# Optimization experiments

Hardware: AMD Instinct MI355X
Metric: run time of the kernel (lower is better)

## Reference

```python
import jax, jax.numpy as jnp
import numpy as np

D = 4096          # input_dims
P = 1             # p in Get_Atten_map_mc
NUM_IMG = 16
N_PER = 64        # objects per image
R_PER = 512       # relations per image
LN_EPS = 1e-5


def _linear_params(key, out_dim, in_dim):
    kw, kb = jax.random.split(key)
    w = jax.random.normal(kw, (out_dim, in_dim), jnp.float32) * 0.02
    b = jax.random.normal(kb, (out_dim,), jnp.float32) * 0.02
    return w, b


def setup_inputs() -> dict:
    key = jax.random.key(0)
    ks = jax.random.split(key, 12)
    N = NUM_IMG * N_PER
    R = NUM_IMG * R_PER

    obj_feats = jax.random.normal(ks[0], (N, D), jnp.float32)
    phr_feats = jax.random.normal(ks[1], (R, D), jnp.float32)

    # im_inds: uniform N_PER objects per image
    im_inds = jnp.repeat(jnp.arange(NUM_IMG, dtype=jnp.int64), N_PER)

    # rel_inds: [img_idx, subj_global, obj_global], R_PER rels per image,
    # subject/object indices local-to-image then offset to global ids.
    subj_loc = jax.random.randint(ks[2], (NUM_IMG, R_PER), 0, N_PER)
    obj_loc = jax.random.randint(ks[3], (NUM_IMG, R_PER), 0, N_PER)
    offs = (jnp.arange(NUM_IMG) * N_PER)[:, None]
    img_col = jnp.repeat(jnp.arange(NUM_IMG), R_PER)
    rel_inds = jnp.stack(
        [img_col, (subj_loc + offs).reshape(-1), (obj_loc + offs).reshape(-1)], axis=1
    ).astype(jnp.int64)

    Ws_w, Ws_b = _linear_params(ks[4], D, D)       # ws
    Wo_w, Wo_b = _linear_params(ks[5], D, D)       # wo
    Ww_w, Ww_b = _linear_params(ks[6], P, D)       # w (attention logits)
    Wc_w, Wc_b = _linear_params(ks[7], D // 2, D)  # conv Linear
    Wt1_w, Wt1_b = _linear_params(ks[8], D // 4, D)
    Wt2_w, Wt2_b = _linear_params(ks[9], D, D // 4)
    ln_g = jnp.ones((D // 4,), jnp.float32)
    ln_b = jnp.zeros((D // 4,), jnp.float32)

    return {
        "obj_feats": obj_feats, "phr_feats": phr_feats,
        "im_inds": im_inds, "rel_inds": rel_inds, "num_img": NUM_IMG,
        "Ws_w": Ws_w, "Ws_b": Ws_b, "Wo_w": Wo_w, "Wo_b": Wo_b,
        "Ww_w": Ww_w, "Ww_b": Ww_b, "Wc_w": Wc_w, "Wc_b": Wc_b,
        "Wt1_w": Wt1_w, "Wt1_b": Wt1_b, "ln_g": ln_g, "ln_b": ln_b,
        "Wt2_w": Wt2_w, "Wt2_b": Wt2_b,
    }


def reference(obj_feats, phr_feats, im_inds, rel_inds, num_img,
              Ws_w, Ws_b, Wo_w, Wo_b, Ww_w, Ww_b, Wc_w, Wc_b,
              Wt1_w, Wt1_b, ln_g, ln_b, Wt2_w, Wt2_b):
    N, d = obj_feats.shape
    n_per = N // num_img
    R = rel_inds.shape[0]
    r_per = R // num_img
    p = Ww_w.shape[0]

    # ws/wo projections over all objects (original recomputes them per image
    # on the full obj_feats -- identical math, computed once here).
    ws_all = obj_feats @ Ws_w.T + Ws_b
    wo_all = obj_feats @ Wo_w.T + Wo_b

    subj = rel_inds[:, 1]
    objc = rel_inds[:, 2]
    prod = ws_all[subj] * wo_all[objc]               # [R, D]
    atten_f = (prod * phr_feats) @ Ww_w.T + Ww_b     # [R, p]

    # conv on object features
    conv_all = jax.nn.relu(obj_feats @ Wc_w.T + Wc_b)  # [N, D/2]

    subj_i = subj.reshape(num_img, r_per)
    objc_i = objc.reshape(num_img, r_per)
    af_i = atten_f.reshape(num_img, r_per, p)
    conv_i = conv_all.reshape(num_img, n_per, -1)

    self_mask = 1.0 - jnp.eye(n_per, dtype=jnp.float32)[:, :, None]  # [n,n,1]

    def per_image(s, o, af, conv_feats):
        head = jnp.minimum(s.min(), o.min())
        A = jnp.zeros((n_per, n_per, p), jnp.float32).at[s - head, o - head].add(af)
        A = jax.nn.sigmoid(A) * self_mask
        A = A / A.sum(1)                               # [n,n,p] / [n,p] (col-normalize)
        A2 = jnp.concatenate([A, A.transpose(1, 0, 2)], axis=-1)  # [n,n,2p]
        # mc_matmul: concat of per-channel mm -> channel-major reshape
        return jnp.einsum('ijc,jd->icd', A2, conv_feats).reshape(n_per, -1)

    ctx = jax.vmap(per_image)(subj_i, objc_i, af_i, conv_i)  # [num_img, n, 2p*D/2]
    ctx = ctx.reshape(N, -1)                                  # [N, D]

    # trans: Linear -> LayerNorm -> ReLU -> Linear
    h = ctx @ Wt1_w.T + Wt1_b
    mu = h.mean(-1, keepdims=True)
    var = ((h - mu) ** 2).mean(-1, keepdims=True)
    h = (h - mu) * jax.lax.rsqrt(var + LN_EPS) * ln_g + ln_b
    h = jax.nn.relu(h)
    out = h @ Wt2_w.T + Wt2_b

    return jax.nn.relu(obj_feats + out)
```

## Files before the change

### kernel.cpp

```cpp
#include <hip/hip_runtime.h>
#include <hip/hip_bf16.h>
#include <math.h>

#define D_   4096
#define NIMG 16
#define NPER 64
#define RPER 512
#define NTOT 1024
#define RTOT 8192
#define DC   2048
#define DT   1024
#define LDW  8192

typedef __attribute__((ext_vector_type(4))) float f32x4;
typedef __attribute__((ext_vector_type(8))) short bf16x8;

#define GLD16(gp, lp) __builtin_amdgcn_global_load_lds( \
    (const __attribute__((address_space(1))) unsigned int*)(gp), \
    (__attribute__((address_space(3))) unsigned int*)(lp), 16, 0, 0)

template<int N> __device__ __forceinline__ void waitvm() {
    asm volatile("s_waitcnt vmcnt(%0)" :: "n"(N) : "memory");
}

__device__ __forceinline__ void fma4(float4& d, float s, const float4 c) {
    d.x = fmaf(s, c.x, d.x); d.y = fmaf(s, c.y, d.y);
    d.z = fmaf(s, c.z, d.z); d.w = fmaf(s, c.w, d.w);
}
__device__ __forceinline__ void st4bf(__hip_bfloat16* p, float4 v) {
    union { __hip_bfloat16 h[4]; ushort4 u; } cv;
    cv.h[0] = __float2bfloat16(v.x); cv.h[1] = __float2bfloat16(v.y);
    cv.h[2] = __float2bfloat16(v.z); cv.h[3] = __float2bfloat16(v.w);
    *(ushort4*)p = cv.u;
}
__device__ __forceinline__ float bf2f(ushort u) {
    union { float f; unsigned int i; } c; c.i = (unsigned int)u << 16; return c.f;
}

__global__ __launch_bounds__(256) void cast_all(
    const float* __restrict__ obj, __hip_bfloat16* __restrict__ obj_bf,
    const float* __restrict__ Ws, const float* __restrict__ Wo,
    const float* __restrict__ Wc, __hip_bfloat16* __restrict__ wbuf,
    const float* __restrict__ Wt1, __hip_bfloat16* __restrict__ wt1r,
    const float* __restrict__ Wt2, __hip_bfloat16* __restrict__ wt2b,
    const float* __restrict__ b0, const float* __restrict__ b1,
    const float* __restrict__ b2, float* __restrict__ cb)
{
    const int b = blockIdx.x;
    const int t = threadIdx.x;
    if (b >= 26624) {
        const int i = (b - 26624) * 256 + t;
        float v;
        if (i < 4096) v = b0[i];
        else if (i < 8192) v = b1[i - 4096];
        else v = b2[i - 8192];
        cb[i] = v;
        return;
    }
    const float* s; __hip_bfloat16* d;
    if (b < 2048)       { s = obj + (size_t)b * 2048;            d = obj_bf + (size_t)b * 2048; }
    else if (b < 10240) { const int rb = b - 2048;  s = Ws + (size_t)rb * 2048; d = wbuf + (size_t)rb * 2048; }
    else if (b < 18432) { const int rb = b - 10240; s = Wo + (size_t)rb * 2048; d = wbuf + 16777216 + (size_t)rb * 2048; }
    else if (b < 22528) { const int rb = b - 18432; s = Wc + (size_t)rb * 2048; d = wbuf + 33554432 + (size_t)rb * 2048; }
    else if (b < 24576) { const int r = b - 22528;
                          s = Wt1 + (size_t)(r & 1023) * 4096 + (r >> 10) * 2048;
                          d = wt1r + (size_t)r * 2048; }
    else                { const int rb = b - 24576; s = Wt2 + (size_t)rb * 2048; d = wt2b + (size_t)rb * 2048; }
    const int i = t * 8;
    float4 v0 = *(const float4*)(s + i);
    float4 v1 = *(const float4*)(s + i + 4);
    union { __hip_bfloat16 h[8]; ushort4 u[2]; } cv;
    cv.h[0] = __float2bfloat16(v0.x); cv.h[1] = __float2bfloat16(v0.y);
    cv.h[2] = __float2bfloat16(v0.z); cv.h[3] = __float2bfloat16(v0.w);
    cv.h[4] = __float2bfloat16(v1.x); cv.h[5] = __float2bfloat16(v1.y);
    cv.h[6] = __float2bfloat16(v1.z); cv.h[7] = __float2bfloat16(v1.w);
    *(ushort4*)(d + i)     = cv.u[0];
    *(ushort4*)(d + i + 4) = cv.u[1];
}

template<int BM, int BN>
__global__ __launch_bounds__(256) void gemm_p2(
    const ushort* __restrict__ A, const ushort* __restrict__ B,
    const float* __restrict__ bias, const float* __restrict__ resid,
    float* __restrict__ C, __hip_bfloat16* __restrict__ C2,
    __hip_bfloat16* __restrict__ C3,
    int M, int K, int ldc, int mode)
{
    constexpr int MREP = BM / 32;
    constexpr int NREP = BN / 32;
    constexpr int SLOTS = (BM + BN) * 4;
    constexpr int NPW = SLOTS / 256;
    constexpr int BUFE = SLOTS * 8;

    __shared__ ushort lds[3][BUFE];

    const int t = threadIdx.x;
    const int lane = t & 63;
    const int wid = t >> 6;
    const int wr = wid >> 1, wc = wid & 1;

    const int MT = M / BM;
    const int G = gridDim.x;
    const int bid = blockIdx.x;
    const int wgid = (bid & 7) * (G >> 3) + (bid >> 3);
    const int nt = wgid / MT, mt = wgid % MT;
    const int bm = mt * BM, bn = nt * BN;

    const ushort* gp[NPW];
    int loff[NPW];
#pragma unroll
    for (int i = 0; i < NPW; ++i) {
        const int slot = i * 256 + t;
        const bool isA = slot < BM * 4;
        const int s2 = isA ? slot : slot - BM * 4;
        const int row = s2 >> 2;
        const int q = (s2 & 3) ^ ((row >> 1) & 3);
        gp[i] = (isA ? A + (size_t)(bm + row) * K : B + (size_t)(bn + row) * K) + q * 8;
        loff[i] = slot * 8;
    }

    auto stage = [&](int b, int kpos) {
#pragma unroll
        for (int i = 0; i < NPW; ++i) GLD16(gp[i] + kpos, &lds[b][loff[i]]);
    };

    int aoff[MREP], boff[NREP];
    const int sx = (((lane >> 4) ^ ((lane >> 1) & 3))) << 3;
#pragma unroll
    for (int m = 0; m < MREP; ++m)
        aoff[m] = (wr * (BM / 2) + (lane & 15) + m * 16) * 32 + sx;
#pragma unroll
    for (int n = 0; n < NREP; ++n)
        boff[n] = BM * 32 + (wc * (BN / 2) + (lane & 15) + n * 16) * 32 + sx;

    f32x4 acc[MREP][NREP] = {};

    const int NT = K >> 5;
    stage(0, 0);
    stage(1, 32);
    if constexpr (NPW == 2) waitvm<2>();
    else if constexpr (NPW == 3) waitvm<3>();
    else waitvm<4>();
    __builtin_amdgcn_sched_barrier(0);
    __builtin_amdgcn_s_barrier();
    __builtin_amdgcn_sched_barrier(0);

    for (int tt = 0; tt < NT; ++tt) {
        const bool pf = (tt + 2 < NT);
        if (pf) stage((tt + 2) % 3, (tt + 2) << 5);
        __builtin_amdgcn_sched_barrier(0);

        const ushort* lb = lds[tt % 3];
        bf16x8 af[MREP], bfv[NREP];
#pragma unroll
        for (int m = 0; m < MREP; ++m) af[m] = *(const bf16x8*)(lb + aoff[m]);
#pragma unroll
        for (int n = 0; n < NREP; ++n) bfv[n] = *(const bf16x8*)(lb + boff[n]);
#pragma unroll
        for (int m = 0; m < MREP; ++m)
#pragma unroll
            for (int n = 0; n < NREP; ++n)
                acc[m][n] = __builtin_amdgcn_mfma_f32_16x16x32_bf16(
                    af[m], bfv[n], acc[m][n], 0, 0, 0);

        __builtin_amdgcn_sched_barrier(0);
        if (pf) {
            if constexpr (NPW == 2) waitvm<2>();
            else if constexpr (NPW == 3) waitvm<3>();
            else waitvm<4>();
        } else {
            waitvm<0>();
        }
        __builtin_amdgcn_sched_barrier(0);
        __builtin_amdgcn_s_barrier();
        __builtin_amdgcn_sched_barrier(0);
    }

    const int col0 = bn + wc * (BN / 2) + (lane & 15);
    const int row0 = bm + wr * (BM / 2) + ((lane >> 4) << 2);
#pragma unroll
    for (int m = 0; m < MREP; ++m) {
#pragma unroll
        for (int n = 0; n < NREP; ++n) {
            const int cn = col0 + n * 16;
            const float bz = bias ? bias[cn] : 0.f;
#pragma unroll
            for (int rg = 0; rg < 4; ++rg) {
                const int gm = row0 + m * 16 + rg;
                float v = acc[m][n][rg] + bz;
                if (mode == 2) {
                    C[(size_t)gm * ldc + cn] = fmaxf(v + resid[(size_t)gm * ldc + cn], 0.f);
                } else if (mode == 4) {
                    if (cn < 8192)
                        C2[(size_t)gm * LDW + cn] = __float2bfloat16(v);
                    else
                        C3[(size_t)gm * 2048 + (cn - 8192)] =
                            __float2bfloat16(fmaxf(v, 0.f));
                } else {
                    C[(size_t)gm * ldc + cn] = v;
                }
            }
        }
    }
}

__global__ __launch_bounds__(256) void atten_kernel(
    const ushort* __restrict__ wswo, const float* __restrict__ phr,
    const int* __restrict__ rel, const float* __restrict__ Www,
    const float* __restrict__ Wwb, float* __restrict__ atten)
{
    const int r = blockIdx.x;
    const int s = rel[r * 3 + 1], o = rel[r * 3 + 2];
    const int t = threadIdx.x;
    const ushort* pws = wswo + (size_t)s * LDW;
    const ushort* pwo = wswo + (size_t)o * LDW + 4096;
    const float*  pph = phr + (size_t)r * D_;
    float sum = 0.f;
#pragma unroll
    for (int half = 0; half < 2; ++half) {
        const int q = t * 8 + half * 2048;
        ushort4 w0 = *(const ushort4*)(pws + q);
        ushort4 w1 = *(const ushort4*)(pws + q + 4);
        ushort4 u0 = *(const ushort4*)(pwo + q);
        ushort4 u1 = *(const ushort4*)(pwo + q + 4);
        float4 p0 = *(const float4*)(pph + q);
        float4 p1 = *(const float4*)(pph + q + 4);
        float4 g0 = *(const float4*)(Www + q);
        float4 g1 = *(const float4*)(Www + q + 4);
        sum += bf2f(w0.x) * bf2f(u0.x) * p0.x * g0.x
             + bf2f(w0.y) * bf2f(u0.y) * p0.y * g0.y
             + bf2f(w0.z) * bf2f(u0.z) * p0.z * g0.z
             + bf2f(w0.w) * bf2f(u0.w) * p0.w * g0.w
             + bf2f(w1.x) * bf2f(u1.x) * p1.x * g1.x
             + bf2f(w1.y) * bf2f(u1.y) * p1.y * g1.y
             + bf2f(w1.z) * bf2f(u1.z) * p1.z * g1.z
             + bf2f(w1.w) * bf2f(u1.w) * p1.w * g1.w;
    }
    for (int off = 32; off > 0; off >>= 1) sum += __shfl_down(sum, off);
    __shared__ float red[4];
    if ((t & 63) == 0) red[t >> 6] = sum;
    __syncthreads();
    if (t == 0) atten[r] = red[0] + red[1] + red[2] + red[3] + Wwb[0];
}

__global__ __launch_bounds__(256) void build_A(
    const int* __restrict__ rel, const float* __restrict__ atten,
    float* __restrict__ Anorm)
{
    const int g = blockIdx.x;
    const int t = threadIdx.x;
    __shared__ float Am[64][64];
    __shared__ float S[64];
    __shared__ int headSh;
    for (int i = t; i < 4096; i += 256) ((float*)Am)[i] = 0.f;
    if (t == 0) headSh = 0x7fffffff;

    int lmin = 0x7fffffff;
    for (int rr = t; rr < RPER; rr += 256) {
        const int base = (g * RPER + rr) * 3;
        lmin = min(lmin, min(rel[base + 1], rel[base + 2]));
    }
    for (int off = 32; off > 0; off >>= 1) lmin = min(lmin, __shfl_down(lmin, off));
    __syncthreads();
    if ((t & 63) == 0) atomicMin(&headSh, lmin);
    __syncthreads();
    const int head = headSh;

    for (int rr = t; rr < RPER; rr += 256) {
        const int base = (g * RPER + rr) * 3;
        atomicAdd(&Am[rel[base + 1] - head][rel[base + 2] - head],
                  atten[g * RPER + rr]);
    }
    __syncthreads();

    for (int idx = t; idx < 4096; idx += 256) {
        const int i = idx >> 6, j = idx & 63;
        float v = 1.f / (1.f + expf(-Am[i][j]));
        if (i == j) v = 0.f;
        Am[i][j] = v;
    }
    __syncthreads();

    if (t < 64) {
        float sum = 0.f;
        for (int k = 0; k < 64; ++k) sum += Am[t][k];
        S[t] = sum;
    }
    __syncthreads();

    float* outg = Anorm + (size_t)g * 4096;
    for (int idx = t; idx < 4096; idx += 256) {
        const int j = idx & 63;
        outg[idx] = ((const float*)Am)[idx] / S[j];
    }
}

__global__ __launch_bounds__(256) void amult_ln(
    const float* __restrict__ Anorm, const float* __restrict__ P,
    const float* __restrict__ w1b, const float* __restrict__ gamma,
    const float* __restrict__ beta, __hip_bfloat16* __restrict__ hb)
{
    const int g = blockIdx.x >> 6;
    const int i = blockIdx.x & 63;
    const int t = threadIdx.x;
    __shared__ float Ar[64], Ac[64];
    if (t < 64) Ar[t] = Anorm[(size_t)g * 4096 + i * 64 + t];
    else if (t < 128) { const int j = t - 64; Ac[j] = Anorm[(size_t)g * 4096 + j * 64 + i]; }
    __syncthreads();

    const float* pg = P + (size_t)g * 64 * 2048;
    float4 v = {0, 0, 0, 0};
    for (int j = 0; j < 64; ++j) {
        float4 p1 = *(const float4*)(pg + (size_t)j * 2048 + (t << 2));
        float4 p2 = *(const float4*)(pg + (size_t)j * 2048 + 1024 + (t << 2));
        fma4(v, Ar[j], p1);
        fma4(v, Ac[j], p2);
    }
    float4 b0 = *(const float4*)(w1b + (t << 2));
    v.x += b0.x; v.y += b0.y; v.z += b0.z; v.w += b0.w;

    float s  = v.x + v.y + v.z + v.w;
    float ss = v.x * v.x + v.y * v.y + v.z * v.z + v.w * v.w;
    for (int off = 32; off > 0; off >>= 1) {
        s  += __shfl_down(s, off);
        ss += __shfl_down(ss, off);
    }
    __shared__ float rs[4], rss[4];
    if ((t & 63) == 0) { rs[t >> 6] = s; rss[t >> 6] = ss; }
    __syncthreads();
    const float tot  = rs[0] + rs[1] + rs[2] + rs[3];
    const float tot2 = rss[0] + rss[1] + rss[2] + rss[3];
    const float mu   = tot * (1.f / DT);
    const float var  = tot2 * (1.f / DT) - mu * mu;
    const float rstd = rsqrtf(var + 1e-5f);
    float4 g4 = *(const float4*)(gamma + (t << 2));
    float4 b4 = *(const float4*)(beta + (t << 2));
    float4 o;
    o.x = fmaxf(fmaf((v.x - mu) * rstd, g4.x, b4.x), 0.f);
    o.y = fmaxf(fmaf((v.y - mu) * rstd, g4.y, b4.y), 0.f);
    o.z = fmaxf(fmaf((v.z - mu) * rstd, g4.z, b4.z), 0.f);
    o.w = fmaxf(fmaf((v.w - mu) * rstd, g4.w, b4.w), 0.f);
    st4bf(hb + (size_t)(g * 64 + i) * DT + (t << 2), o);
}

extern "C" void kernel_launch(void* const* d_in, const int* in_sizes, int n_in,
                              void* d_out, int out_size, void* d_ws, size_t ws_size,
                              hipStream_t stream)
{
    const float* obj   = (const float*)d_in[0];
    const float* phr   = (const float*)d_in[1];
    const int*   rel   = (const int*)d_in[3];
    const float* Ws_w  = (const float*)d_in[5];
    const float* Ws_b  = (const float*)d_in[6];
    const float* Wo_w  = (const float*)d_in[7];
    const float* Wo_b  = (const float*)d_in[8];
    const float* Ww_w  = (const float*)d_in[9];
    const float* Ww_b  = (const float*)d_in[10];
    const float* Wc_w  = (const float*)d_in[11];
    const float* Wc_b  = (const float*)d_in[12];
    const float* Wt1_w = (const float*)d_in[13];
    const float* Wt1_b = (const float*)d_in[14];
    const float* ln_g  = (const float*)d_in[15];
    const float* ln_b  = (const float*)d_in[16];
    const float* Wt2_w = (const float*)d_in[17];
    const float* Wt2_b = (const float*)d_in[18];
    float* out = (float*)d_out;

    float* ws = (float*)d_ws;
    __hip_bfloat16* wbuf    = (__hip_bfloat16*)ws;
    __hip_bfloat16* h_bf    = (__hip_bfloat16*)ws;
    __hip_bfloat16* obj_bf  = (__hip_bfloat16*)(ws + 20971520);
    float* Pbuf             = ws + 20971520;
    __hip_bfloat16* wswo_bf = (__hip_bfloat16*)(ws + 23068672);
    __hip_bfloat16* conv_bf = (__hip_bfloat16*)(ws + 27262976);
    __hip_bfloat16* wt1r    = (__hip_bfloat16*)(ws + 28311552);
    __hip_bfloat16* wt2b    = (__hip_bfloat16*)(ws + 30408704);
    float* atten  = ws + 32505856;
    float* Anorm  = ws + 32514048;
    float* cbias  = ws + 32579584;

    const dim3 blk(256);

    cast_all<<<dim3(26664), blk, 0, stream>>>(
        obj, obj_bf, Ws_w, Wo_w, Wc_w, wbuf, Wt1_w, wt1r, Wt2_w, wt2b,
        Ws_b, Wo_b, Wc_b, cbias);

    gemm_p2<128, 128><<<dim3(640), blk, 0, stream>>>(
        (const ushort*)obj_bf, (const ushort*)wbuf, cbias, nullptr,
        nullptr, wswo_bf, conv_bf, NTOT, D_, 0, 4);

    atten_kernel<<<dim3(RTOT), blk, 0, stream>>>(
        (const ushort*)wswo_bf, phr, rel, Ww_w, Ww_b, atten);
    build_A<<<dim3(NIMG), blk, 0, stream>>>(rel, atten, Anorm);

    gemm_p2<64, 64><<<dim3(512), blk, 0, stream>>>(
        (const ushort*)conv_bf, (const ushort*)wt1r, nullptr, nullptr,
        Pbuf, nullptr, nullptr, NTOT, DC, DC, 0);

    amult_ln<<<dim3(1024), blk, 0, stream>>>(Anorm, Pbuf, Wt1_b, ln_g, ln_b, h_bf);

    gemm_p2<64, 128><<<dim3(512), blk, 0, stream>>>(
        (const ushort*)h_bf, (const ushort*)wt2b, Wt2_b, obj,
        out, nullptr, nullptr, NTOT, DT, D_, 2);
}
```

Before: 299.1 us.

## Stage mode-4 GEMM epilogue through LDS for vectorized bf16 stores; remap blocks across XCDs

In the fused GEMM's mode-4 epilogue, each wave writes its bias-added (and ReLU'd) bf16 tile into a padded LDS patch, then reads it back row-wise and writes 16-byte vectors to global memory instead of scattered 2-byte stores. The atten and amult_ln kernels remap blockIdx so consecutive relation/image work lands on the same XCD (mod-8 interleave), aiming for better L2 locality on the gathered rows. The LDS staging reuses the GEMM's LDS buffer and assumes it is large enough and no longer needed. The XCD remap assumes round-robin dispatch across 8 XCDs.

```diff
diff --git a/kernel.cpp b/kernel.cpp
--- a/kernel.cpp
+++ b/kernel.cpp
@@ -35,6 +35,9 @@
 }
 __device__ __forceinline__ float bf2f(ushort u) {
     union { float f; unsigned int i; } c; c.i = (unsigned int)u << 16; return c.f;
+}
+__device__ __forceinline__ ushort f2bfu(float v) {
+    union { __hip_bfloat16 h; ushort u; } c; c.h = __float2bfloat16(v); return c.u;
 }
 
 __global__ __launch_bounds__(256) void cast_all(
@@ -178,6 +181,43 @@
 
     const int col0 = bn + wc * (BN / 2) + (lane & 15);
     const int row0 = bm + wr * (BM / 2) + ((lane >> 4) << 2);
+
+    if (mode == 4) {
+        ushort* patch = ((ushort*)lds) + wid * (64 * 72);
+        const bool doRelu = (bn >= 8192);
+#pragma unroll
+        for (int m = 0; m < MREP; ++m) {
+#pragma unroll
+            for (int n = 0; n < NREP; ++n) {
+                const float bz = bias[col0 + n * 16];
+#pragma unroll
+                for (int rg = 0; rg < 4; ++rg) {
+                    float v = acc[m][n][rg] + bz;
+                    if (doRelu) v = fmaxf(v, 0.f);
+                    const int lr = m * 16 + ((lane >> 4) << 2) + rg;
+                    const int lc = n * 16 + (lane & 15);
+                    patch[lr * 72 + lc] = f2bfu(v);
+                }
+            }
+        }
+        const int lcol8 = (lane & 7) * 8;
+        const int gcol = bn + wc * (BN / 2) + lcol8;
+#pragma unroll
+        for (int m = 0; m < MREP; ++m) {
+#pragma unroll
+            for (int pass = 0; pass < 2; ++pass) {
+                const int lr = m * 16 + pass * 8 + (lane >> 3);
+                uint4 v4 = *(const uint4*)(patch + lr * 72 + lcol8);
+                const int grow = bm + wr * (BM / 2) + lr;
+                if (gcol < 8192)
+                    *(uint4*)((ushort*)C2 + (size_t)grow * LDW + gcol) = v4;
+                else
+                    *(uint4*)((ushort*)C3 + (size_t)grow * 2048 + (gcol - 8192)) = v4;
+            }
+        }
+        return;
+    }
+
 #pragma unroll
     for (int m = 0; m < MREP; ++m) {
 #pragma unroll
@@ -188,17 +228,9 @@
             for (int rg = 0; rg < 4; ++rg) {
                 const int gm = row0 + m * 16 + rg;
                 float v = acc[m][n][rg] + bz;
-                if (mode == 2) {
-                    C[(size_t)gm * ldc + cn] = fmaxf(v + resid[(size_t)gm * ldc + cn], 0.f);
-                } else if (mode == 4) {
-                    if (cn < 8192)
-                        C2[(size_t)gm * LDW + cn] = __float2bfloat16(v);
-                    else
-                        C3[(size_t)gm * 2048 + (cn - 8192)] =
-                            __float2bfloat16(fmaxf(v, 0.f));
-                } else {
-                    C[(size_t)gm * ldc + cn] = v;
-                }
+                if (mode == 2)
+                    v = fmaxf(v + resid[(size_t)gm * ldc + cn], 0.f);
+                C[(size_t)gm * ldc + cn] = v;
             }
         }
     }
@@ -209,7 +241,7 @@
     const int* __restrict__ rel, const float* __restrict__ Www,
     const float* __restrict__ Wwb, float* __restrict__ atten)
 {
-    const int r = blockIdx.x;
+    const int r = (blockIdx.x & 7) * 1024 + (blockIdx.x >> 3);
     const int s = rel[r * 3 + 1], o = rel[r * 3 + 2];
     const int t = threadIdx.x;
     const ushort* pws = wswo + (size_t)s * LDW;
@@ -300,8 +332,9 @@
     const float* __restrict__ w1b, const float* __restrict__ gamma,
     const float* __restrict__ beta, __hip_bfloat16* __restrict__ hb)
 {
-    const int g = blockIdx.x >> 6;
-    const int i = blockIdx.x & 63;
+    const int wg = (blockIdx.x & 7) * 128 + (blockIdx.x >> 3);
+    const int g = wg >> 6;
+    const int i = wg & 63;
     const int t = threadIdx.x;
     __shared__ float Ar[64], Ac[64];
     if (t < 64) Ar[t] = Anorm[(size_t)g * 4096 + i * 64 + t];
```

After: 289.8 us. 1.03x faster.
